# Performance work log

Hardware: AMD Instinct MI355X
Metric: run time of the kernel (lower is better)

## Reference

```python
import jax, jax.numpy as jnp
import numpy as np

N, E, F_IN, H, C, N_CLS = 50000, 800000, 128, 4, 32, 10
NEG_SLOPE = 0.2


def setup_inputs() -> dict:
    key = jax.random.key(0)
    ks = jax.random.split(key, 24)
    d = {}
    d["x"] = jax.random.normal(ks[0], (N, F_IN), jnp.float32)
    d["edge_index"] = jax.random.randint(ks[1], (2, E), 0, N, jnp.int32)

    def lin(k, fan_in, shape):
        return jax.random.normal(k, shape, jnp.float32) / np.float32(np.sqrt(fan_in))

    # conv1: F_IN -> H*C, heads H, concat
    d["W1"]  = lin(ks[2], F_IN, (F_IN, H * C))
    d["a1s"] = lin(ks[3], C, (H, C))
    d["a1d"] = lin(ks[4], C, (H, C))
    d["b1"]  = jnp.zeros((H * C,), jnp.float32)
    d["lin1_W"] = lin(ks[5], F_IN, (F_IN, H * C))
    d["lin1_b"] = jnp.zeros((H * C,), jnp.float32)
    # conv2: H*C -> H*C
    d["W2"]  = lin(ks[6], H * C, (H * C, H * C))
    d["a2s"] = lin(ks[7], C, (H, C))
    d["a2d"] = lin(ks[8], C, (H, C))
    d["b2"]  = jnp.zeros((H * C,), jnp.float32)
    d["lin2_W"] = lin(ks[9], H * C, (H * C, H * C))
    d["lin2_b"] = jnp.zeros((H * C,), jnp.float32)
    # conv3: H*C -> N_CLS, heads H, concat=False (mean over heads)
    d["W3"]  = lin(ks[10], H * C, (H * C, H * N_CLS))
    d["a3s"] = lin(ks[11], N_CLS, (H, N_CLS))
    d["a3d"] = lin(ks[12], N_CLS, (H, N_CLS))
    d["b3"]  = jnp.zeros((N_CLS,), jnp.float32)
    d["lin3_W"] = lin(ks[13], H * C, (H * C, N_CLS))
    d["lin3_b"] = jnp.zeros((N_CLS,), jnp.float32)
    return d


def gat_conv(x, src, dst, W, a_s, a_d, b, heads, out_ch, concat):
    n = x.shape[0]
    h = (x @ W).reshape(n, heads, out_ch)                # [N,H,C]
    alpha_src = jnp.sum(h * a_s, axis=-1)                # [N,H]
    alpha_dst = jnp.sum(h * a_d, axis=-1)                # [N,H]
    e = jax.nn.leaky_relu(alpha_src[src] + alpha_dst[dst], NEG_SLOPE)  # [E,H]
    # segment softmax over edges grouped by destination node
    m = jax.ops.segment_max(e, dst, num_segments=n)      # [N,H]
    p = jnp.exp(e - m[dst])
    denom = jax.ops.segment_sum(p, dst, num_segments=n)  # [N,H]
    alpha = p / (denom[dst] + 1e-16)                     # [E,H]
    out = jax.ops.segment_sum(alpha[:, :, None] * h[src], dst, num_segments=n)  # [N,H,C]
    out = out.reshape(n, heads * out_ch) if concat else out.mean(axis=1)
    return out + b


def reference(x, edge_index, W1, a1s, a1d, b1, lin1_W, lin1_b,
              W2, a2s, a2d, b2, lin2_W, lin2_b,
              W3, a3s, a3d, b3, lin3_W, lin3_b):
    n = x.shape[0]
    # PyG GATConv adds self-loops by default
    loops = jnp.arange(n, dtype=edge_index.dtype)
    src = jnp.concatenate([edge_index[0], loops])
    dst = jnp.concatenate([edge_index[1], loops])

    x = jax.nn.elu(gat_conv(x, src, dst, W1, a1s, a1d, b1, H, C, True) + x @ lin1_W + lin1_b)
    x = jax.nn.elu(gat_conv(x, src, dst, W2, a2s, a2d, b2, H, C, True) + x @ lin2_W + lin2_b)
    x = gat_conv(x, src, dst, W3, a3s, a3d, b3, H, N_CLS, False) + x @ lin3_W + lin3_b
    return x
```

## Files before the change

### kernel.cpp

```cpp
#include <hip/hip_runtime.h>
#include <math.h>


#define HEADS 4

typedef __attribute__((ext_vector_type(8))) short short8v;
typedef __attribute__((ext_vector_type(4))) float float4v;

__device__ __forceinline__ float lrelu(float v) { return v > 0.f ? v : 0.2f * v; }

__device__ __forceinline__ unsigned short f2bf(float f) {
    unsigned u = __float_as_uint(f);
    unsigned r = u + 0x7FFFu + ((u >> 16) & 1u);
    return (unsigned short)(r >> 16);
}
__device__ __forceinline__ float bf2f(unsigned short u) {
    return __uint_as_float(((unsigned)u) << 16);
}

__global__ void castX(const float* __restrict__ x, unsigned short* __restrict__ xb, int n4) {
    int i = blockIdx.x * blockDim.x + threadIdx.x;
    if (i >= n4) return;
    float4 v = *(const float4*)&x[(size_t)i * 4];
    ushort4 o;
    o.x = f2bf(v.x); o.y = f2bf(v.y); o.z = f2bf(v.z); o.w = f2bf(v.w);
    *(ushort4*)&xb[(size_t)i * 4] = o;
}

__global__ void packB12(const float* __restrict__ W, const float* __restrict__ LW,
                        const float* __restrict__ a_s, const float* __restrict__ a_d,
                        unsigned short* __restrict__ BT) {
    int i = blockIdx.x * blockDim.x + threadIdx.x;
    if (i >= 320 * 128) return;
    int m = i >> 7, k = i & 127;
    float v = 0.f;
    if (m < 128) {
        v = W[(size_t)k * 128 + m];
    } else if (m < 256) {
        v = LW[(size_t)k * 128 + (m - 128)];
    } else if (m < 260) {
        int h = m - 256;
        for (int c = 0; c < 32; ++c)
            v = fmaf(W[(size_t)k * 128 + h * 32 + c], a_s[h * 32 + c], v);
    } else if (m < 264) {
        int h = m - 260;
        for (int c = 0; c < 32; ++c)
            v = fmaf(W[(size_t)k * 128 + h * 32 + c], a_d[h * 32 + c], v);
    }
    BT[i] = f2bf(v);
}

__global__ void packB3(const float* __restrict__ W3, const float* __restrict__ LW3,
                       const float* __restrict__ a_s, const float* __restrict__ a_d,
                       unsigned short* __restrict__ BT) {
    int i = blockIdx.x * blockDim.x + threadIdx.x;
    if (i >= 128 * 128) return;
    int m = i >> 7, k = i & 127;
    float v = 0.f;
    if (m < 40) {
        v = W3[(size_t)k * 40 + m];
    } else if (m < 50) {
        v = LW3[(size_t)k * 10 + (m - 40)];
    } else if (m >= 64 && m < 68) {
        int h = m - 64;
        for (int c = 0; c < 10; ++c)
            v = fmaf(W3[(size_t)k * 40 + h * 10 + c], a_s[h * 10 + c], v);
    } else if (m >= 68 && m < 72) {
        int h = m - 68;
        for (int c = 0; c < 10; ++c)
            v = fmaf(W3[(size_t)k * 40 + h * 10 + c], a_d[h * 10 + c], v);
    }
    BT[i] = f2bf(v);
}

__global__ __launch_bounds__(256) void mfma_gemm(const unsigned short* __restrict__ A,
                                                 const unsigned short* __restrict__ BT,
                                                 unsigned short* __restrict__ C,
                                                 float* __restrict__ asrc,
                                                 float* __restrict__ adst,
                                                 int nrows, int Mc) {
    const int wave = threadIdx.x >> 6;
    const int lane = threadIdx.x & 63;
    const int row0 = blockIdx.y * 64 + wave * 16;
    const int col0 = blockIdx.x * 64;
    const int lrow = lane & 15;
    const int kgrp = lane >> 4;
    const bool alphaBlk = (col0 >= Mc);

    float4v acc0 = {0.f, 0.f, 0.f, 0.f};
    float4v acc1 = {0.f, 0.f, 0.f, 0.f};
    float4v acc2 = {0.f, 0.f, 0.f, 0.f};
    float4v acc3 = {0.f, 0.f, 0.f, 0.f};

    int arow = row0 + lrow;
    if (arow >= nrows) arow = nrows - 1;
    const unsigned short* Ap = A + (size_t)arow * 128 + kgrp * 8;
    const unsigned short* Bp = BT + (size_t)(col0 + lrow) * 128 + kgrp * 8;

    if (alphaBlk) {
#pragma unroll
        for (int t = 0; t < 4; ++t) {
            short8v a  = *(const short8v*)(Ap + t * 32);
            short8v b0 = *(const short8v*)(Bp + t * 32);
            acc0 = __builtin_amdgcn_mfma_f32_16x16x32_bf16(a, b0, acc0, 0, 0, 0);
        }
        if (lrow < 8) {
            float* dst = (lrow < 4) ? asrc : adst;
            int hh = lrow & 3;
#pragma unroll
            for (int r = 0; r < 4; ++r) {
                int row = row0 + kgrp * 4 + r;
                if (row < nrows) dst[(size_t)row * 4 + hh] = acc0[r];
            }
        }
        return;
    }

#pragma unroll
    for (int t = 0; t < 4; ++t) {
        short8v a  = *(const short8v*)(Ap + t * 32);
        short8v b0 = *(const short8v*)(Bp + t * 32);
        short8v b1 = *(const short8v*)(Bp + 16 * 128 + t * 32);
        short8v b2 = *(const short8v*)(Bp + 32 * 128 + t * 32);
        short8v b3 = *(const short8v*)(Bp + 48 * 128 + t * 32);
        acc0 = __builtin_amdgcn_mfma_f32_16x16x32_bf16(a, b0, acc0, 0, 0, 0);
        acc1 = __builtin_amdgcn_mfma_f32_16x16x32_bf16(a, b1, acc1, 0, 0, 0);
        acc2 = __builtin_amdgcn_mfma_f32_16x16x32_bf16(a, b2, acc2, 0, 0, 0);
        acc3 = __builtin_amdgcn_mfma_f32_16x16x32_bf16(a, b3, acc3, 0, 0, 0);
    }

#pragma unroll
    for (int r = 0; r < 4; ++r) {
        int row = row0 + kgrp * 4 + r;
        if (row >= nrows) continue;
        size_t base = (size_t)row * Mc + col0 + lrow;
        C[base]      = f2bf(acc0[r]);
        C[base + 16] = f2bf(acc1[r]);
        C[base + 32] = f2bf(acc2[r]);
        C[base + 48] = f2bf(acc3[r]);
    }
}

__global__ void deg_hist4(const int* __restrict__ dst, int E, int* __restrict__ deg) {
    int e = (blockIdx.x * blockDim.x + threadIdx.x) * 4;
    if (e + 3 < E) {
        int4 d = *(const int4*)&dst[e];
        atomicAdd(&deg[d.x], 1);
        atomicAdd(&deg[d.y], 1);
        atomicAdd(&deg[d.z], 1);
        atomicAdd(&deg[d.w], 1);
    } else {
        for (; e < E; ++e) atomicAdd(&deg[dst[e]], 1);
    }
}

__global__ void scan_block(const int* __restrict__ in, int* __restrict__ out,
                           int* __restrict__ bsum, int n) {
    __shared__ int tmp[256];
    int i = blockIdx.x * 256 + threadIdx.x;
    int v = (i < n) ? in[i] + 1 : 0;
    tmp[threadIdx.x] = v;
    __syncthreads();
    for (int d = 1; d < 256; d <<= 1) {
        int t = (threadIdx.x >= d) ? tmp[threadIdx.x - d] : 0;
        __syncthreads();
        tmp[threadIdx.x] += t;
        __syncthreads();
    }
    if (i < n) out[i] = tmp[threadIdx.x] - v;
    if (threadIdx.x == 255) bsum[blockIdx.x] = tmp[255];
}

__global__ void scan_bsum(int* bsum, int nb) {
    __shared__ int tmp[256];
    int v = (threadIdx.x < nb) ? bsum[threadIdx.x] : 0;
    tmp[threadIdx.x] = v;
    __syncthreads();
    for (int d = 1; d < 256; d <<= 1) {
        int t = (threadIdx.x >= d) ? tmp[threadIdx.x - d] : 0;
        __syncthreads();
        tmp[threadIdx.x] += t;
        __syncthreads();
    }
    if (threadIdx.x < nb) bsum[threadIdx.x] = tmp[threadIdx.x] - v;
}

__global__ void scan_add(int* out, const int* __restrict__ bsum, int n) {
    int i = blockIdx.x * 256 + threadIdx.x;
    if (i < n) out[i] += bsum[blockIdx.x];
}

#define FILL_U 8
__global__ __launch_bounds__(256) void csr_fill_bucket(
    const int* __restrict__ ei, int E, int N,
    const int* __restrict__ rowptr, int* __restrict__ cur,
    int2* __restrict__ adjdst)
{
    const int bucket = blockIdx.x & 7;
    const int grp    = blockIdx.x >> 3;
    const int ngrp   = gridDim.x >> 3;
    const int npb    = (N + 7) >> 3;
    const int lo = bucket * npb;
    const int hi = (lo + npb < N) ? lo + npb : N;

    for (int i = lo + grp * 256 + (int)threadIdx.x; i < hi; i += ngrp * 256)
        adjdst[rowptr[i]] = make_int2(i, i);

    const int chunkSz = 256 * FILL_U;
    const int nchunks = (E + chunkSz - 1) / chunkSz;
    const int* dstRow = ei + E;
    for (int c = grp; c < nchunks; c += ngrp) {
        int base = c * chunkSz + (int)threadIdx.x;
#pragma unroll
        for (int k = 0; k < FILL_U; ++k) {
            int e = base + k * 256;
            if (e < E) {
                int d = dstRow[e];
                if (d >= lo && d < hi) {
                    int s = ei[e];
                    int pos = rowptr[d] + 1 + atomicAdd(&cur[d], 1);
                    adjdst[pos] = make_int2(s, d);
                }
            }
        }
    }
}

__global__ void edge_w(const int2* __restrict__ adjdst, int ET,
                       const float* __restrict__ asrc,
                       const float* __restrict__ adst, float* __restrict__ P) {
    int j = blockIdx.x * blockDim.x + threadIdx.x;
    if (j >= ET) return;
    int2 sd = adjdst[j];
    float4 av = *(const float4*)&asrc[(size_t)sd.x * 4];
    float4 dv = *(const float4*)&adst[(size_t)sd.y * 4];
    float4 p;
    p.x = __expf(lrelu(av.x + dv.x));
    p.y = __expf(lrelu(av.y + dv.y));
    p.z = __expf(lrelu(av.z + dv.z));
    p.w = __expf(lrelu(av.w + dv.w));
    *(float4*)&P[(size_t)j * 4] = p;
}

__global__ __launch_bounds__(256) void gat_gather128(
    const int* __restrict__ rowptr, const int2* __restrict__ adjdst, int ET,
    const float* __restrict__ P, const unsigned short* __restrict__ Hb,
    const float* __restrict__ bias, const float* __restrict__ lbias,
    unsigned short* __restrict__ xout, int n)
{
    int node = (blockIdx.x * 256 + threadIdx.x) >> 6;
    int lane = threadIdx.x & 63;
    if (node >= n) return;
    int beg = rowptr[node];
    int end = (node + 1 < n) ? rowptr[node + 1] : ET;

    int ep = lane >> 4;
    int q  = lane & 15;
    int c0 = q * 8;
    int h  = q >> 2;

    float accp = 0.f;
    float a[8];
#pragma unroll
    for (int k = 0; k < 8; ++k) a[k] = 0.f;

    int j = beg + ep;
    int sN = 0; float pN = 0.f;
    bool valid = j < end;
    if (valid) { sN = adjdst[j].x; pN = P[(size_t)j * 4 + h]; }
    while (valid) {
        int s = sN; float p = pN;
        int j2 = j + 4;
        bool v2 = j2 < end;
        if (v2) { sN = adjdst[j2].x; pN = P[(size_t)j2 * 4 + h]; }
        short8v hv = *(const short8v*)&Hb[(size_t)s * 256 + c0];
        accp += p;
#pragma unroll
        for (int k = 0; k < 8; ++k)
            a[k] = fmaf(p, bf2f((unsigned short)hv[k]), a[k]);
        j = j2; valid = v2;
    }
#pragma unroll
    for (int off = 16; off <= 32; off <<= 1) {
        accp += __shfl_xor(accp, off);
#pragma unroll
        for (int k = 0; k < 8; ++k) a[k] += __shfl_xor(a[k], off);
    }

    if (ep == 0) {
        float inv = 1.f / (accp + 1e-16f);
        short8v lv = *(const short8v*)&Hb[(size_t)node * 256 + 128 + c0];
        unsigned short w[8];
#pragma unroll
        for (int k = 0; k < 8; ++k) {
            float v = a[k] * inv + bias[c0 + k] + bf2f((unsigned short)lv[k]) + lbias[c0 + k];
            v = v > 0.f ? v : __expf(v) - 1.f;
            w[k] = f2bf(v);
        }
        *(short8v*)&xout[(size_t)node * 128 + c0] = *(short8v*)w;
    }
}

__global__ __launch_bounds__(256) void gat_gather40(
    const int* __restrict__ rowptr, const int2* __restrict__ adjdst, int ET,
    const float* __restrict__ P, const unsigned short* __restrict__ Hb3,
    const float* __restrict__ bias, const float* __restrict__ lbias,
    float* __restrict__ out, int n)
{
    int node = (blockIdx.x * 256 + threadIdx.x) >> 6;
    int lane = threadIdx.x & 63;
    if (node >= n) return;
    int beg = rowptr[node];
    int end = (node + 1 < n) ? rowptr[node + 1] : ET;

    int ep  = lane >> 5;
    int sub = lane & 31;
    int act = sub < 20;
    int c0  = act ? sub * 2 : 0;
    int h   = act ? (sub / 5) : 0;

    float accp = 0.f, a0 = 0.f, a1 = 0.f;
    int j = beg + ep;
    int sN = 0; float pN = 0.f;
    bool valid = j < end;
    if (valid) { sN = adjdst[j].x; pN = P[(size_t)j * 4 + h]; }
    while (valid) {
        int s = sN; float p = pN;
        int j2 = j + 2;
        bool v2 = j2 < end;
        if (v2) { sN = adjdst[j2].x; pN = P[(size_t)j2 * 4 + h]; }
        ushort2 hv = *(const ushort2*)&Hb3[(size_t)s * 64 + c0];
        accp += p;
        a0 = fmaf(p, bf2f(hv.x), a0);
        a1 = fmaf(p, bf2f(hv.y), a1);
        j = j2; valid = v2;
    }
    accp += __shfl_xor(accp, 32);
    a0   += __shfl_xor(a0, 32);
    a1   += __shfl_xor(a1, 32);

    float inv = 0.25f / (accp + 1e-16f);
    a0 *= inv;
    a1 *= inv;

    float r = 0.f;
#pragma unroll
    for (int hh = 0; hh < 4; ++hh) {
        int ch = hh * 10 + lane;
        float lo = __shfl(a0, ch >> 1);
        float hi = __shfl(a1, ch >> 1);
        r += (ch & 1) ? hi : lo;
    }
    if (lane < 10) {
        size_t o = (size_t)node * 10 + lane;
        float lin = bf2f(Hb3[(size_t)node * 64 + 40 + lane]);
        out[o] = r + bias[lane] + lin + lbias[lane];
    }
}

extern "C" void kernel_launch(void* const* d_in, const int* in_sizes, int n_in,
                              void* d_out, int out_size, void* d_ws, size_t ws_size,
                              hipStream_t stream) {
    const float* x   = (const float*)d_in[0];
    const int*   ei  = (const int*)d_in[1];
    const float* W1  = (const float*)d_in[2];
    const float* a1s = (const float*)d_in[3];
    const float* a1d = (const float*)d_in[4];
    const float* b1  = (const float*)d_in[5];
    const float* l1W = (const float*)d_in[6];
    const float* l1b = (const float*)d_in[7];
    const float* W2  = (const float*)d_in[8];
    const float* a2s = (const float*)d_in[9];
    const float* a2d = (const float*)d_in[10];
    const float* b2  = (const float*)d_in[11];
    const float* l2W = (const float*)d_in[12];
    const float* l2b = (const float*)d_in[13];
    const float* W3  = (const float*)d_in[14];
    const float* a3s = (const float*)d_in[15];
    const float* a3d = (const float*)d_in[16];
    const float* b3  = (const float*)d_in[17];
    const float* l3W = (const float*)d_in[18];
    const float* l3b = (const float*)d_in[19];

    const int N  = in_sizes[0] / 128;
    const int E  = in_sizes[1] / 2;
    const int ET = E + N;

    unsigned short* Xb = (unsigned short*)d_ws;
    unsigned short* Hb = Xb + (size_t)N * 128;
    unsigned short* BT = Hb + (size_t)N * 256;
    float* asrc = (float*)(BT + 320 * 128);
    float* adst = asrc + (size_t)N * 4;
    float* P    = adst + (size_t)N * 4;
    int* deg    = (int*)(P + (size_t)ET * 4);
    int* cur    = deg + N;
    int* rowptr = cur + N;
    int* bsum   = rowptr + N;
    int2* adjdst = (int2*)(bsum + 256);

    const int nScanBlocks = (N + 255) / 256;
    int etBlocks   = (ET + 255) / 256;
    int waveBlocks = (N * 64 + 255) / 256;
    int rowBlocks  = (N + 63) / 64;

    hipMemsetAsync(deg, 0, (size_t)N * 2 * 4, stream);
    deg_hist4<<<(E / 4 + 256) / 256, 256, 0, stream>>>(ei + E, E, deg);
    scan_block<<<nScanBlocks, 256, 0, stream>>>(deg, rowptr, bsum, N);
    scan_bsum<<<1, 256, 0, stream>>>(bsum, nScanBlocks);
    scan_add<<<nScanBlocks, 256, 0, stream>>>(rowptr, bsum, N);
    csr_fill_bucket<<<512, 256, 0, stream>>>(ei, E, N, rowptr, cur, adjdst);

    castX<<<(N * 32 + 255) / 256, 256, 0, stream>>>(x, Xb, N * 32);

    packB12<<<(320 * 128 + 255) / 256, 256, 0, stream>>>(W1, l1W, a1s, a1d, BT);
    mfma_gemm<<<dim3(5, rowBlocks), 256, 0, stream>>>(Xb, BT, Hb, asrc, adst, N, 256);
    edge_w<<<etBlocks, 256, 0, stream>>>(adjdst, ET, asrc, adst, P);
    gat_gather128<<<waveBlocks, 256, 0, stream>>>(rowptr, adjdst, ET, P, Hb, b1, l1b, Xb, N);

    packB12<<<(320 * 128 + 255) / 256, 256, 0, stream>>>(W2, l2W, a2s, a2d, BT);
    mfma_gemm<<<dim3(5, rowBlocks), 256, 0, stream>>>(Xb, BT, Hb, asrc, adst, N, 256);
    edge_w<<<etBlocks, 256, 0, stream>>>(adjdst, ET, asrc, adst, P);
    gat_gather128<<<waveBlocks, 256, 0, stream>>>(rowptr, adjdst, ET, P, Hb, b2, l2b, Xb, N);

    packB3<<<(128 * 128 + 255) / 256, 256, 0, stream>>>(W3, l3W, a3s, a3d, BT);
    mfma_gemm<<<dim3(2, rowBlocks), 256, 0, stream>>>(Xb, BT, Hb, asrc, adst, N, 64);
    edge_w<<<etBlocks, 256, 0, stream>>>(adjdst, ET, asrc, adst, P);
    gat_gather40<<<waveBlocks, 256, 0, stream>>>(rowptr, adjdst, ET, P, Hb, b3, l3b, (float*)d_out, N);
}
```

Baseline: 341.5 us.

## Fuse edge-weight computation into gather kernels and compact CSR adjacency to int

Drops the separate edge_w kernel and the materialised per-edge P buffer. Each gather kernel now computes exp(leaky_relu(asrc+adst)) inline from a source index list that holds only int sources instead of int2 pairs. Layer 3 output is stored in a padded head-interleaved 80-wide layout so gat_gather40 can use 16-byte loads with 8 edges in flight per wave. The CSR fill also uses a larger grid with a smaller unroll. The cost removed is three passes writing and reading 4 floats per edge, paid for with redundant exp work in the gather threads.

```diff
diff --git a/kernel.cpp b/kernel.cpp
--- a/kernel.cpp
+++ b/kernel.cpp
@@ -78,7 +78,8 @@
                                                  unsigned short* __restrict__ C,
                                                  float* __restrict__ asrc,
                                                  float* __restrict__ adst,
-                                                 int nrows, int Mc) {
+                                                 int nrows, int Mc, int Cstride,
+                                                 int permStore) {
     const int wave = threadIdx.x >> 6;
     const int lane = threadIdx.x & 63;
     const int row0 = blockIdx.y * 64 + wave * 16;
@@ -87,10 +88,7 @@
     const int kgrp = lane >> 4;
     const bool alphaBlk = (col0 >= Mc);
 
-    float4v acc0 = {0.f, 0.f, 0.f, 0.f};
-    float4v acc1 = {0.f, 0.f, 0.f, 0.f};
-    float4v acc2 = {0.f, 0.f, 0.f, 0.f};
-    float4v acc3 = {0.f, 0.f, 0.f, 0.f};
+    float4v acc[4] = {{0.f,0.f,0.f,0.f},{0.f,0.f,0.f,0.f},{0.f,0.f,0.f,0.f},{0.f,0.f,0.f,0.f}};
 
     int arow = row0 + lrow;
     if (arow >= nrows) arow = nrows - 1;
@@ -102,7 +100,7 @@
         for (int t = 0; t < 4; ++t) {
             short8v a  = *(const short8v*)(Ap + t * 32);
             short8v b0 = *(const short8v*)(Bp + t * 32);
-            acc0 = __builtin_amdgcn_mfma_f32_16x16x32_bf16(a, b0, acc0, 0, 0, 0);
+            acc[0] = __builtin_amdgcn_mfma_f32_16x16x32_bf16(a, b0, acc[0], 0, 0, 0);
         }
         if (lrow < 8) {
             float* dst = (lrow < 4) ? asrc : adst;
@@ -110,7 +108,7 @@
 #pragma unroll
             for (int r = 0; r < 4; ++r) {
                 int row = row0 + kgrp * 4 + r;
-                if (row < nrows) dst[(size_t)row * 4 + hh] = acc0[r];
+                if (row < nrows) dst[(size_t)row * 4 + hh] = acc[0][r];
             }
         }
         return;
@@ -118,26 +116,35 @@
 
 #pragma unroll
     for (int t = 0; t < 4; ++t) {
-        short8v a  = *(const short8v*)(Ap + t * 32);
-        short8v b0 = *(const short8v*)(Bp + t * 32);
-        short8v b1 = *(const short8v*)(Bp + 16 * 128 + t * 32);
-        short8v b2 = *(const short8v*)(Bp + 32 * 128 + t * 32);
-        short8v b3 = *(const short8v*)(Bp + 48 * 128 + t * 32);
-        acc0 = __builtin_amdgcn_mfma_f32_16x16x32_bf16(a, b0, acc0, 0, 0, 0);
-        acc1 = __builtin_amdgcn_mfma_f32_16x16x32_bf16(a, b1, acc1, 0, 0, 0);
-        acc2 = __builtin_amdgcn_mfma_f32_16x16x32_bf16(a, b2, acc2, 0, 0, 0);
-        acc3 = __builtin_amdgcn_mfma_f32_16x16x32_bf16(a, b3, acc3, 0, 0, 0);
+        short8v a = *(const short8v*)(Ap + t * 32);
+#pragma unroll
+        for (int kk = 0; kk < 4; ++kk) {
+            short8v b = *(const short8v*)(Bp + kk * 16 * 128 + t * 32);
+            acc[kk] = __builtin_amdgcn_mfma_f32_16x16x32_bf16(a, b, acc[kk], 0, 0, 0);
+        }
     }
 
 #pragma unroll
     for (int r = 0; r < 4; ++r) {
         int row = row0 + kgrp * 4 + r;
         if (row >= nrows) continue;
-        size_t base = (size_t)row * Mc + col0 + lrow;
-        C[base]      = f2bf(acc0[r]);
-        C[base + 16] = f2bf(acc1[r]);
-        C[base + 32] = f2bf(acc2[r]);
-        C[base + 48] = f2bf(acc3[r]);
+        if (!permStore) {
+            size_t base = (size_t)row * Cstride + col0 + lrow;
+            C[base]      = f2bf(acc[0][r]);
+            C[base + 16] = f2bf(acc[1][r]);
+            C[base + 32] = f2bf(acc[2][r]);
+            C[base + 48] = f2bf(acc[3][r]);
+        } else {
+#pragma unroll
+            for (int kk = 0; kk < 4; ++kk) {
+                int col = lrow + kk * 16;
+                int pos;
+                if (col < 40)      pos = (col / 5) * 8 + (col % 5);
+                else if (col < 50) pos = 64 + (col - 40);
+                else continue;
+                C[(size_t)row * 80 + pos] = f2bf(acc[kk][r]);
+            }
+        }
     }
 }
 
@@ -190,11 +197,11 @@
     if (i < n) out[i] += bsum[blockIdx.x];
 }
 
-#define FILL_U 8
+#define FILL_U 4
 __global__ __launch_bounds__(256) void csr_fill_bucket(
     const int* __restrict__ ei, int E, int N,
     const int* __restrict__ rowptr, int* __restrict__ cur,
-    int2* __restrict__ adjdst)
+    int* __restrict__ adj)
 {
     const int bucket = blockIdx.x & 7;
     const int grp    = blockIdx.x >> 3;
@@ -204,7 +211,7 @@
     const int hi = (lo + npb < N) ? lo + npb : N;
 
     for (int i = lo + grp * 256 + (int)threadIdx.x; i < hi; i += ngrp * 256)
-        adjdst[rowptr[i]] = make_int2(i, i);
+        adj[rowptr[i]] = i;
 
     const int chunkSz = 256 * FILL_U;
     const int nchunks = (E + chunkSz - 1) / chunkSz;
@@ -217,34 +224,18 @@
             if (e < E) {
                 int d = dstRow[e];
                 if (d >= lo && d < hi) {
-                    int s = ei[e];
                     int pos = rowptr[d] + 1 + atomicAdd(&cur[d], 1);
-                    adjdst[pos] = make_int2(s, d);
+                    adj[pos] = ei[e];
                 }
             }
         }
     }
 }
 
-__global__ void edge_w(const int2* __restrict__ adjdst, int ET,
-                       const float* __restrict__ asrc,
-                       const float* __restrict__ adst, float* __restrict__ P) {
-    int j = blockIdx.x * blockDim.x + threadIdx.x;
-    if (j >= ET) return;
-    int2 sd = adjdst[j];
-    float4 av = *(const float4*)&asrc[(size_t)sd.x * 4];
-    float4 dv = *(const float4*)&adst[(size_t)sd.y * 4];
-    float4 p;
-    p.x = __expf(lrelu(av.x + dv.x));
-    p.y = __expf(lrelu(av.y + dv.y));
-    p.z = __expf(lrelu(av.z + dv.z));
-    p.w = __expf(lrelu(av.w + dv.w));
-    *(float4*)&P[(size_t)j * 4] = p;
-}
-
 __global__ __launch_bounds__(256) void gat_gather128(
-    const int* __restrict__ rowptr, const int2* __restrict__ adjdst, int ET,
-    const float* __restrict__ P, const unsigned short* __restrict__ Hb,
+    const int* __restrict__ rowptr, const int* __restrict__ adj, int ET,
+    const float* __restrict__ asrc, const float* __restrict__ adst,
+    const unsigned short* __restrict__ Hb,
     const float* __restrict__ bias, const float* __restrict__ lbias,
     unsigned short* __restrict__ xout, int n)
 {
@@ -258,6 +249,7 @@
     int q  = lane & 15;
     int c0 = q * 8;
     int h  = q >> 2;
+    float adh = adst[(size_t)node * 4 + h];
 
     float accp = 0.f;
     float a[8];
@@ -265,14 +257,15 @@
     for (int k = 0; k < 8; ++k) a[k] = 0.f;
 
     int j = beg + ep;
-    int sN = 0; float pN = 0.f;
     bool valid = j < end;
-    if (valid) { sN = adjdst[j].x; pN = P[(size_t)j * 4 + h]; }
+    int sN = 0; float avN = 0.f;
+    if (valid) { sN = adj[j]; avN = asrc[(size_t)sN * 4 + h]; }
     while (valid) {
-        int s = sN; float p = pN;
+        int s = sN; float av = avN;
         int j2 = j + 4;
         bool v2 = j2 < end;
-        if (v2) { sN = adjdst[j2].x; pN = P[(size_t)j2 * 4 + h]; }
+        if (v2) { sN = adj[j2]; avN = asrc[(size_t)sN * 4 + h]; }
+        float p = __expf(lrelu(av + adh));
         short8v hv = *(const short8v*)&Hb[(size_t)s * 256 + c0];
         accp += p;
 #pragma unroll
@@ -302,8 +295,9 @@
 }
 
 __global__ __launch_bounds__(256) void gat_gather40(
-    const int* __restrict__ rowptr, const int2* __restrict__ adjdst, int ET,
-    const float* __restrict__ P, const unsigned short* __restrict__ Hb3,
+    const int* __restrict__ rowptr, const int* __restrict__ adj, int ET,
+    const float* __restrict__ asrc, const float* __restrict__ adst,
+    const unsigned short* __restrict__ Hb3,
     const float* __restrict__ bias, const float* __restrict__ lbias,
     float* __restrict__ out, int n)
 {
@@ -313,48 +307,55 @@
     int beg = rowptr[node];
     int end = (node + 1 < n) ? rowptr[node + 1] : ET;
 
-    int ep  = lane >> 5;
-    int sub = lane & 31;
-    int act = sub < 20;
-    int c0  = act ? sub * 2 : 0;
-    int h   = act ? (sub / 5) : 0;
-
-    float accp = 0.f, a0 = 0.f, a1 = 0.f;
-    int j = beg + ep;
-    int sN = 0; float pN = 0.f;
+    int slot = lane >> 3;
+    int sub  = lane & 7;
+    int h    = sub >> 1;
+    float adh = adst[(size_t)node * 4 + h];
+
+    float accp = 0.f;
+    float a[5];
+#pragma unroll
+    for (int k = 0; k < 5; ++k) a[k] = 0.f;
+
+    int j = beg + slot;
     bool valid = j < end;
-    if (valid) { sN = adjdst[j].x; pN = P[(size_t)j * 4 + h]; }
+    int sN = 0; float avN = 0.f;
+    if (valid) { sN = adj[j]; avN = asrc[(size_t)sN * 4 + h]; }
     while (valid) {
-        int s = sN; float p = pN;
-        int j2 = j + 2;
+        int s = sN; float av = avN;
+        int j2 = j + 8;
         bool v2 = j2 < end;
-        if (v2) { sN = adjdst[j2].x; pN = P[(size_t)j2 * 4 + h]; }
-        ushort2 hv = *(const ushort2*)&Hb3[(size_t)s * 64 + c0];
+        if (v2) { sN = adj[j2]; avN = asrc[(size_t)sN * 4 + h]; }
+        float p = __expf(lrelu(av + adh));
+        short8v hv = *(const short8v*)&Hb3[(size_t)s * 80 + sub * 8];
         accp += p;
-        a0 = fmaf(p, bf2f(hv.x), a0);
-        a1 = fmaf(p, bf2f(hv.y), a1);
+#pragma unroll
+        for (int k = 0; k < 5; ++k)
+            a[k] = fmaf(p, bf2f((unsigned short)hv[k]), a[k]);
         j = j2; valid = v2;
     }
-    accp += __shfl_xor(accp, 32);
-    a0   += __shfl_xor(a0, 32);
-    a1   += __shfl_xor(a1, 32);
-
+#pragma unroll
+    for (int off = 8; off <= 32; off <<= 1) {
+        accp += __shfl_xor(accp, off);
+#pragma unroll
+        for (int k = 0; k < 5; ++k) a[k] += __shfl_xor(a[k], off);
+    }
     float inv = 0.25f / (accp + 1e-16f);
-    a0 *= inv;
-    a1 *= inv;
-
-    float r = 0.f;
-#pragma unroll
-    for (int hh = 0; hh < 4; ++hh) {
-        int ch = hh * 10 + lane;
-        float lo = __shfl(a0, ch >> 1);
-        float hi = __shfl(a1, ch >> 1);
-        r += (ch & 1) ? hi : lo;
-    }
-    if (lane < 10) {
-        size_t o = (size_t)node * 10 + lane;
-        float lin = bf2f(Hb3[(size_t)node * 64 + 40 + lane]);
-        out[o] = r + bias[lane] + lin + lbias[lane];
+#pragma unroll
+    for (int k = 0; k < 5; ++k) a[k] *= inv;
+#pragma unroll
+    for (int off = 2; off <= 4; off <<= 1) {
+#pragma unroll
+        for (int k = 0; k < 5; ++k) a[k] += __shfl_xor(a[k], off);
+    }
+
+    if (lane < 2) {
+        int cc0 = sub * 5;
+#pragma unroll
+        for (int k = 0; k < 5; ++k) {
+            float lin = bf2f(Hb3[(size_t)node * 80 + 64 + cc0 + k]);
+            out[(size_t)node * 10 + cc0 + k] = a[k] + bias[cc0 + k] + lin + lbias[cc0 + k];
+        }
     }
 }
 
@@ -391,15 +392,13 @@
     unsigned short* BT = Hb + (size_t)N * 256;
     float* asrc = (float*)(BT + 320 * 128);
     float* adst = asrc + (size_t)N * 4;
-    float* P    = adst + (size_t)N * 4;
-    int* deg    = (int*)(P + (size_t)ET * 4);
+    int* deg    = (int*)(adst + (size_t)N * 4);
     int* cur    = deg + N;
     int* rowptr = cur + N;
     int* bsum   = rowptr + N;
-    int2* adjdst = (int2*)(bsum + 256);
+    int* adj    = bsum + 256;
 
     const int nScanBlocks = (N + 255) / 256;
-    int etBlocks   = (ET + 255) / 256;
     int waveBlocks = (N * 64 + 255) / 256;
     int rowBlocks  = (N + 63) / 64;
 
@@ -408,22 +407,19 @@
     scan_block<<<nScanBlocks, 256, 0, stream>>>(deg, rowptr, bsum, N);
     scan_bsum<<<1, 256, 0, stream>>>(bsum, nScanBlocks);
     scan_add<<<nScanBlocks, 256, 0, stream>>>(rowptr, bsum, N);
-    csr_fill_bucket<<<512, 256, 0, stream>>>(ei, E, N, rowptr, cur, adjdst);
+    csr_fill_bucket<<<4096, 256, 0, stream>>>(ei, E, N, rowptr, cur, adj);
 
     castX<<<(N * 32 + 255) / 256, 256, 0, stream>>>(x, Xb, N * 32);
 
     packB12<<<(320 * 128 + 255) / 256, 256, 0, stream>>>(W1, l1W, a1s, a1d, BT);
-    mfma_gemm<<<dim3(5, rowBlocks), 256, 0, stream>>>(Xb, BT, Hb, asrc, adst, N, 256);
-    edge_w<<<etBlocks, 256, 0, stream>>>(adjdst, ET, asrc, adst, P);
-    gat_gather128<<<waveBlocks, 256, 0, stream>>>(rowptr, adjdst, ET, P, Hb, b1, l1b, Xb, N);
+    mfma_gemm<<<dim3(5, rowBlocks), 256, 0, stream>>>(Xb, BT, Hb, asrc, adst, N, 256, 256, 0);
+    gat_gather128<<<waveBlocks, 256, 0, stream>>>(rowptr, adj, ET, asrc, adst, Hb, b1, l1b, Xb, N);
 
     packB12<<<(320 * 128 + 255) / 256, 256, 0, stream>>>(W2, l2W, a2s, a2d, BT);
-    mfma_gemm<<<dim3(5, rowBlocks), 256, 0, stream>>>(Xb, BT, Hb, asrc, adst, N, 256);
-    edge_w<<<etBlocks, 256, 0, stream>>>(adjdst, ET, asrc, adst, P);
-    gat_gather128<<<waveBlocks, 256, 0, stream>>>(rowptr, adjdst, ET, P, Hb, b2, l2b, Xb, N);
+    mfma_gemm<<<dim3(5, rowBlocks), 256, 0, stream>>>(Xb, BT, Hb, asrc, adst, N, 256, 256, 0);
+    gat_gather128<<<waveBlocks, 256, 0, stream>>>(rowptr, adj, ET, asrc, adst, Hb, b2, l2b, Xb, N);
 
     packB3<<<(128 * 128 + 255) / 256, 256, 0, stream>>>(W3, l3W, a3s, a3d, BT);
-    mfma_gemm<<<dim3(2, rowBlocks), 256, 0, stream>>>(Xb, BT, Hb, asrc, adst, N, 64);
-    edge_w<<<etBlocks, 256, 0, stream>>>(adjdst, ET, asrc, adst, P);
-    gat_gather40<<<waveBlocks, 256, 0, stream>>>(rowptr, adjdst, ET, P, Hb, b3, l3b, (float*)d_out, N);
-}
+    mfma_gemm<<<dim3(2, rowBlocks), 256, 0, stream>>>(Xb, BT, Hb, asrc, adst, N, 64, 80, 1);
+    gat_gather40<<<waveBlocks, 256, 0, stream>>>(rowptr, adj, ET, asrc, adst, Hb, b3, l3b, (float*)d_out, N);
+}
```

Measured after the change: 321.7 us. 1.06x faster.
